# Kernel optimization log

Hardware: AMD Instinct MI355X
Metric: run time of the kernel (lower is better)

The kernel has to match this reference:

```python
import jax, jax.numpy as jnp
import numpy as np

K = 3  # number of nearest neighbors for interpolation
BIG = 1e10  # masks out cross-batch pairs in the distance matrix


def setup_inputs() -> dict:
    key = jax.random.key(0)
    ks = jax.random.split(key, 8)
    N, Ns, C, Cs, B = 4096, 16384, 256, 128, 4
    Din, H = C + Cs, 256
    return {
        "x": jax.random.normal(ks[0], (N, C), dtype=jnp.float32),
        "pos": jax.random.normal(ks[1], (N, 3), dtype=jnp.float32),
        "batch": jnp.sort(jax.random.randint(ks[2], (N,), 0, B)),
        "x_skip": jax.random.normal(ks[3], (Ns, Cs), dtype=jnp.float32),
        "pos_skip": jax.random.normal(ks[4], (Ns, 3), dtype=jnp.float32),
        "batch_skip": jnp.sort(jax.random.randint(ks[5], (Ns,), 0, B)),
        "W1": jax.random.normal(ks[6], (Din, H), dtype=jnp.float32) * (1.0 / np.sqrt(Din)),
        "b1": jnp.zeros((H,), dtype=jnp.float32),
        "W2": jax.random.normal(ks[7], (H, H), dtype=jnp.float32) * (1.0 / np.sqrt(H)),
        "b2": jnp.zeros((H,), dtype=jnp.float32),
    }


def reference(x, pos, batch, x_skip, pos_skip, batch_skip, W1, b1, W2, b2):
    # knn_interpolate: squared distances from each fine point to all coarse points,
    # masked so neighbors only come from the same batch element.
    d2 = jnp.sum((pos_skip[:, None, :] - pos[None, :, :]) ** 2, axis=-1)  # [Ns, N]
    d2 = jnp.where(batch_skip[:, None] != batch[None, :], BIG, d2)
    neg_d2, idx = jax.lax.top_k(-d2, K)          # k smallest distances, [Ns, K]
    w = 1.0 / jnp.clip(-neg_d2, 1e-16)           # inverse-squared-distance weights
    num = jnp.sum(x[idx] * w[..., None], axis=1)  # [Ns, C] weighted gather-reduce
    y = num / jnp.sum(w, axis=1, keepdims=True)
    # concat skip features, then MLP (Linear-ReLU-Linear-ReLU)
    y = jnp.concatenate([y, x_skip], axis=1)      # [Ns, C + Cs]
    h = jax.nn.relu(y @ W1 + b1)
    out = jax.nn.relu(h @ W2 + b2)
    return (out, pos_skip, batch_skip)
```

## Files before the change

kernel.cpp:

```cpp
#include <hip/hip_runtime.h>
#include <stdint.h>

#define NPTS   4096
#define NSKIP  16384
#define CCH    256
#define CSK    128
#define DIN    384
#define HDIM   256
#define BIGF   1e10f

typedef unsigned short u16;
typedef __attribute__((ext_vector_type(8))) short short8;
typedef __attribute__((ext_vector_type(4))) float floatx4;

__device__ __forceinline__ u16 f2bf(float f) {
    union { float f; uint32_t u; } c; c.f = f;
    uint32_t u = c.u;
    return (u16)((u + 0x7FFFu + ((u >> 16) & 1u)) >> 16);
}

__device__ __forceinline__ double pkkey(float d, int j) {
    return __hiloint2double(__float_as_int(d), j);
}

__global__ __launch_bounds__(256) void prep_kernel(
    const float* __restrict__ W1, const float* __restrict__ W2,
    u16* __restrict__ W1p, u16* __restrict__ W2p,
    const float* __restrict__ pos, float4* __restrict__ pos4,
    const int* __restrict__ batch, int* __restrict__ range)
{
    const int bid = blockIdx.x;
    const int t = threadIdx.x;

    const float* W = (bid < 48) ? W1 : W2;
    u16* Wp       = (bid < 48) ? W1p : W2p;
    const int KT  = (bid < 48) ? 12 : 8;
    const int g   = ((bid < 48) ? bid : (bid - 48)) * 256 + t;

    const int lane = g & 63;
    const int kt = (g >> 6) % KT;
    const int nt = (g >> 6) / KT;
    const int kbase = kt * 32 + (lane >> 4) * 8;
    const int n = nt * 16 + (lane & 15);
    u16 v[8];
#pragma unroll
    for (int j = 0; j < 8; ++j) v[j] = f2bf(W[(size_t)(kbase + j) * HDIM + n]);
#pragma unroll
    for (int j = 0; j < 8; ++j) Wp[(size_t)g * 8 + j] = v[j];

    if (bid >= 48 && bid < 64) {
        const int p = (bid - 48) * 256 + t;
        pos4[p] = make_float4(pos[p * 3 + 0], pos[p * 3 + 1], pos[p * 3 + 2], 0.0f);
    }

    if (bid == 0) {
        for (int j = t * 16; j < t * 16 + 16; ++j) {
            if (j == 0) {
                const int b0 = batch[0];
                for (int b = 0; b <= b0; ++b) range[b] = 0;
            } else {
                const int bp = batch[j - 1], bj = batch[j];
                for (int b = bp + 1; b <= bj; ++b) range[b] = j;
            }
            if (j == NPTS - 1) {
                const int bl = batch[NPTS - 1];
                for (int b = bl + 1; b <= 4; ++b) range[b] = NPTS;
            }
        }
    }
}

__global__ __launch_bounds__(256) void knn_kernel(
    const float4* __restrict__ pos4, const int* __restrict__ range,
    const float* __restrict__ pos_skip, const int* __restrict__ batch_skip,
    int* __restrict__ idx3, float* __restrict__ w3)
{
    const int t = threadIdx.x;
    const int i = blockIdx.x * 8 + (t >> 5);
    const int sub = t & 31;
    const int b = batch_skip[i];
    const int start = range[b], end = range[b + 1];

    const float px = pos_skip[i * 3 + 0];
    const float py = pos_skip[i * 3 + 1];
    const float pz = pos_skip[i * 3 + 2];

    const double BIGKEY = pkkey(BIGF, 0x7FFFFFFF);
    double k0 = BIGKEY, k1 = BIGKEY, k2 = BIGKEY;

    for (int j = start + sub; j < end; j += 32) {
        const float4 q = pos4[j];
        const float dx = __fsub_rn(px, q.x);
        const float dy = __fsub_rn(py, q.y);
        const float dz = __fsub_rn(pz, q.z);
        const float dd = __fadd_rn(__fadd_rn(__fmul_rn(dx, dx), __fmul_rn(dy, dy)),
                                   __fmul_rn(dz, dz));
        const double kk = pkkey(dd, j);
        const double u0 = fmax(k0, kk); k0 = fmin(k0, kk);
        const double u1 = fmax(k1, u0); k1 = fmin(k1, u0);
        k2 = fmin(k2, u1);
    }

#pragma unroll
    for (int m = 1; m < 32; m <<= 1) {
        const double o0 = __shfl_xor(k0, m);
        const double o1 = __shfl_xor(k1, m);
        const double o2 = __shfl_xor(k2, m);
        double u0 = fmax(k0, o0); k0 = fmin(k0, o0);
        double u1 = fmax(k1, u0); k1 = fmin(k1, u0);
        k2 = fmin(k2, u1);
        u1 = fmax(k1, o1); k1 = fmin(k1, o1);
        k2 = fmin(k2, u1);
        k2 = fmin(k2, o2);
    }

    if (sub == 0) {
        const float d0 = __int_as_float(__double2hiint(k0));
        const float d1 = __int_as_float(__double2hiint(k1));
        const float d2 = __int_as_float(__double2hiint(k2));
        const float w0 = 1.0f / fmaxf(d0, 1e-16f);
        const float w1 = 1.0f / fmaxf(d1, 1e-16f);
        const float w2 = 1.0f / fmaxf(d2, 1e-16f);
        const float inv = 1.0f / (w0 + w1 + w2);
        idx3[i * 3 + 0] = __double2loint(k0);
        idx3[i * 3 + 1] = __double2loint(k1);
        idx3[i * 3 + 2] = __double2loint(k2);
        w3[i * 3 + 0] = w0 * inv; w3[i * 3 + 1] = w1 * inv; w3[i * 3 + 2] = w2 * inv;
    }
}

__global__ __launch_bounds__(256) void fused_mlp_kernel(
    const float* __restrict__ x, const float* __restrict__ x_skip,
    const int* __restrict__ idx3, const float* __restrict__ w3,
    const u16* __restrict__ W1p, const float* __restrict__ b1,
    const u16* __restrict__ W2p, const float* __restrict__ b2,
    const float* __restrict__ pos_skip, const int* __restrict__ batch_skip,
    float* __restrict__ out)
{
    __shared__ u16 sA[32 * 392];
    const int t = threadIdx.x;
    const int row0 = blockIdx.x * 32;

#pragma unroll
    for (int k = 0; k < 8; ++k) {
        const int g = t + 256 * k;
        const int row = g >> 6, c4 = g & 63;
        const int R = row0 + row;
        const int i0 = idx3[R * 3 + 0], i1 = idx3[R * 3 + 1], i2 = idx3[R * 3 + 2];
        const float w0 = w3[R * 3 + 0], w1 = w3[R * 3 + 1], w2 = w3[R * 3 + 2];
        const float4 v0 = *(const float4*)(x + (size_t)i0 * CCH + c4 * 4);
        const float4 v1 = *(const float4*)(x + (size_t)i1 * CCH + c4 * 4);
        const float4 v2 = *(const float4*)(x + (size_t)i2 * CCH + c4 * 4);
        const float a  = w0 * v0.x + w1 * v1.x + w2 * v2.x;
        const float bq = w0 * v0.y + w1 * v1.y + w2 * v2.y;
        const float cq = w0 * v0.z + w1 * v1.z + w2 * v2.z;
        const float dq = w0 * v0.w + w1 * v1.w + w2 * v2.w;
        uint2 pk;
        pk.x = (uint32_t)f2bf(a)  | ((uint32_t)f2bf(bq) << 16);
        pk.y = (uint32_t)f2bf(cq) | ((uint32_t)f2bf(dq) << 16);
        *(uint2*)(sA + row * 392 + c4 * 4) = pk;
    }
#pragma unroll
    for (int k = 0; k < 4; ++k) {
        const int g = t + 256 * k;
        const int row = g >> 5, c4 = g & 31;
        const float4 v = *(const float4*)(x_skip + (size_t)(row0 + row) * CSK + c4 * 4);
        uint2 pk;
        pk.x = (uint32_t)f2bf(v.x) | ((uint32_t)f2bf(v.y) << 16);
        pk.y = (uint32_t)f2bf(v.z) | ((uint32_t)f2bf(v.w) << 16);
        *(uint2*)(sA + row * 392 + CCH + c4 * 4) = pk;
    }
    __syncthreads();

    const int wave = t >> 6, lane = t & 63;
    const int quad = lane >> 4, ml = lane & 15;

    floatx4 acc[2][4] = {};
    {
        const u16* aA = sA + ml * 392 + quad * 8;
        for (int kt = 0; kt < 12; ++kt) {
            short8 a0 = *(const short8*)(aA + kt * 32);
            short8 a1 = *(const short8*)(aA + 16 * 392 + kt * 32);
#pragma unroll
            for (int nt = 0; nt < 4; ++nt) {
                const int ntile = wave * 4 + nt;
                short8 bfr = *(const short8*)(W1p + (size_t)((ntile * 12 + kt) * 64 + lane) * 8);
                acc[0][nt] = __builtin_amdgcn_mfma_f32_16x16x32_bf16(a0, bfr, acc[0][nt], 0, 0, 0);
                acc[1][nt] = __builtin_amdgcn_mfma_f32_16x16x32_bf16(a1, bfr, acc[1][nt], 0, 0, 0);
            }
        }
    }
    __syncthreads();

#pragma unroll
    for (int mt = 0; mt < 2; ++mt) {
#pragma unroll
        for (int nt = 0; nt < 4; ++nt) {
            const int n = (wave * 4 + nt) * 16 + ml;
            const float bv = b1[n];
#pragma unroll
            for (int r = 0; r < 4; ++r) {
                const int m = mt * 16 + quad * 4 + r;
                sA[m * 264 + n] = f2bf(fmaxf(acc[mt][nt][r] + bv, 0.0f));
            }
        }
    }
    __syncthreads();

    floatx4 acc2[2][4] = {};
    {
        const u16* aH = sA + ml * 264 + quad * 8;
        for (int kt = 0; kt < 8; ++kt) {
            short8 a0 = *(const short8*)(aH + kt * 32);
            short8 a1 = *(const short8*)(aH + 16 * 264 + kt * 32);
#pragma unroll
            for (int nt = 0; nt < 4; ++nt) {
                const int ntile = wave * 4 + nt;
                short8 bfr = *(const short8*)(W2p + (size_t)((ntile * 8 + kt) * 64 + lane) * 8);
                acc2[0][nt] = __builtin_amdgcn_mfma_f32_16x16x32_bf16(a0, bfr, acc2[0][nt], 0, 0, 0);
                acc2[1][nt] = __builtin_amdgcn_mfma_f32_16x16x32_bf16(a1, bfr, acc2[1][nt], 0, 0, 0);
            }
        }
    }

#pragma unroll
    for (int mt = 0; mt < 2; ++mt) {
#pragma unroll
        for (int nt = 0; nt < 4; ++nt) {
            const int n = (wave * 4 + nt) * 16 + ml;
            const float bv = b2[n];
#pragma unroll
            for (int r = 0; r < 4; ++r) {
                const int m = row0 + mt * 16 + quad * 4 + r;
                out[(size_t)m * HDIM + n] = fmaxf(acc2[mt][nt][r] + bv, 0.0f);
            }
        }
    }

    if (t < 128) {
        const int e = blockIdx.x * 128 + t;
        const size_t base = (size_t)NSKIP * HDIM;
        if (e < NSKIP * 3) out[base + e] = pos_skip[e];
        else               out[base + e] = (float)batch_skip[e - NSKIP * 3];
    }
}

extern "C" void kernel_launch(void* const* d_in, const int* in_sizes, int n_in,
                              void* d_out, int out_size, void* d_ws, size_t ws_size,
                              hipStream_t stream) {
    const float* x         = (const float*)d_in[0];
    const float* pos       = (const float*)d_in[1];
    const int*   batch     = (const int*)d_in[2];
    const float* x_skip    = (const float*)d_in[3];
    const float* pos_skip  = (const float*)d_in[4];
    const int*   batch_skip= (const int*)d_in[5];
    const float* W1        = (const float*)d_in[6];
    const float* b1        = (const float*)d_in[7];
    const float* W2        = (const float*)d_in[8];
    const float* b2        = (const float*)d_in[9];
    float* out = (float*)d_out;

    char* ws = (char*)d_ws;
    u16*    W1p   = (u16*)ws;
    u16*    W2p   = (u16*)(ws + 196608);
    int*    range = (int*)(ws + 327680);
    float4* pos4  = (float4*)(ws + 327712);
    int*    idx3  = (int*)(ws + 393248);
    float*  w3    = (float*)(ws + 589856);

    prep_kernel<<<80, 256, 0, stream>>>(W1, W2, W1p, W2p, pos, pos4, batch, range);
    knn_kernel<<<NSKIP / 8, 256, 0, stream>>>(pos4, range, pos_skip, batch_skip, idx3, w3);
    fused_mlp_kernel<<<NSKIP / 32, 256, 0, stream>>>(x, x_skip, idx3, w3,
                                                     W1p, b1, W2p, b2,
                                                     pos_skip, batch_skip, out);
}
```

Before: 119.7 us.

## Fuse KNN search into MLP kernel with 8 lanes per query

Merges the separate KNN kernel into the fused MLP kernel: each block first finds the 3 nearest coarse points for its 32 rows using 8 lanes per row and stores indices and weights in shared memory, then gathers and runs the MLP. This removes one kernel launch and the global write/read of idx3 and w3. In exchange, each lane now scans four times as many candidates serially and the KNN phase runs with far fewer threads in flight, which may leave it latency-bound.

After: 137.8 us. 15.2% more time.

```diff
diff --git a/kernel.cpp b/kernel.cpp
--- a/kernel.cpp
+++ b/kernel.cpp
@@ -70,84 +70,95 @@
     }
 }
 
-__global__ __launch_bounds__(256) void knn_kernel(
+__global__ __launch_bounds__(256) void knn_fused_kernel(
+    const float* __restrict__ x, const float* __restrict__ x_skip,
     const float4* __restrict__ pos4, const int* __restrict__ range,
-    const float* __restrict__ pos_skip, const int* __restrict__ batch_skip,
-    int* __restrict__ idx3, float* __restrict__ w3)
-{
-    const int t = threadIdx.x;
-    const int i = blockIdx.x * 8 + (t >> 5);
-    const int sub = t & 31;
-    const int b = batch_skip[i];
-    const int start = range[b], end = range[b + 1];
-
-    const float px = pos_skip[i * 3 + 0];
-    const float py = pos_skip[i * 3 + 1];
-    const float pz = pos_skip[i * 3 + 2];
-
-    const double BIGKEY = pkkey(BIGF, 0x7FFFFFFF);
-    double k0 = BIGKEY, k1 = BIGKEY, k2 = BIGKEY;
-
-    for (int j = start + sub; j < end; j += 32) {
-        const float4 q = pos4[j];
-        const float dx = __fsub_rn(px, q.x);
-        const float dy = __fsub_rn(py, q.y);
-        const float dz = __fsub_rn(pz, q.z);
-        const float dd = __fadd_rn(__fadd_rn(__fmul_rn(dx, dx), __fmul_rn(dy, dy)),
-                                   __fmul_rn(dz, dz));
-        const double kk = pkkey(dd, j);
-        const double u0 = fmax(k0, kk); k0 = fmin(k0, kk);
-        const double u1 = fmax(k1, u0); k1 = fmin(k1, u0);
-        k2 = fmin(k2, u1);
-    }
-
-#pragma unroll
-    for (int m = 1; m < 32; m <<= 1) {
-        const double o0 = __shfl_xor(k0, m);
-        const double o1 = __shfl_xor(k1, m);
-        const double o2 = __shfl_xor(k2, m);
-        double u0 = fmax(k0, o0); k0 = fmin(k0, o0);
-        double u1 = fmax(k1, u0); k1 = fmin(k1, u0);
-        k2 = fmin(k2, u1);
-        u1 = fmax(k1, o1); k1 = fmin(k1, o1);
-        k2 = fmin(k2, u1);
-        k2 = fmin(k2, o2);
-    }
-
-    if (sub == 0) {
-        const float d0 = __int_as_float(__double2hiint(k0));
-        const float d1 = __int_as_float(__double2hiint(k1));
-        const float d2 = __int_as_float(__double2hiint(k2));
-        const float w0 = 1.0f / fmaxf(d0, 1e-16f);
-        const float w1 = 1.0f / fmaxf(d1, 1e-16f);
-        const float w2 = 1.0f / fmaxf(d2, 1e-16f);
-        const float inv = 1.0f / (w0 + w1 + w2);
-        idx3[i * 3 + 0] = __double2loint(k0);
-        idx3[i * 3 + 1] = __double2loint(k1);
-        idx3[i * 3 + 2] = __double2loint(k2);
-        w3[i * 3 + 0] = w0 * inv; w3[i * 3 + 1] = w1 * inv; w3[i * 3 + 2] = w2 * inv;
-    }
-}
-
-__global__ __launch_bounds__(256) void fused_mlp_kernel(
-    const float* __restrict__ x, const float* __restrict__ x_skip,
-    const int* __restrict__ idx3, const float* __restrict__ w3,
     const u16* __restrict__ W1p, const float* __restrict__ b1,
     const u16* __restrict__ W2p, const float* __restrict__ b2,
     const float* __restrict__ pos_skip, const int* __restrict__ batch_skip,
     float* __restrict__ out)
 {
     __shared__ u16 sA[32 * 392];
+    __shared__ int   sIdx[32 * 3];
+    __shared__ float sWgt[32 * 3];
     const int t = threadIdx.x;
     const int row0 = blockIdx.x * 32;
+
+#pragma unroll
+    for (int k = 0; k < 4; ++k) {
+        const int g = t + 256 * k;
+        const int row = g >> 5, c4 = g & 31;
+        const float4 v = *(const float4*)(x_skip + (size_t)(row0 + row) * CSK + c4 * 4);
+        uint2 pk;
+        pk.x = (uint32_t)f2bf(v.x) | ((uint32_t)f2bf(v.y) << 16);
+        pk.y = (uint32_t)f2bf(v.z) | ((uint32_t)f2bf(v.w) << 16);
+        *(uint2*)(sA + row * 392 + CCH + c4 * 4) = pk;
+    }
+
+    {
+        const int row_l = t >> 3;
+        const int sub   = t & 7;
+        const int i = row0 + row_l;
+        const int b = batch_skip[i];
+        const int start = range[b], end = range[b + 1];
+
+        const float px = pos_skip[i * 3 + 0];
+        const float py = pos_skip[i * 3 + 1];
+        const float pz = pos_skip[i * 3 + 2];
+
+        const double BIGKEY = pkkey(BIGF, 0x7FFFFFFF);
+        double k0 = BIGKEY, k1 = BIGKEY, k2 = BIGKEY;
+
+        for (int j = start + sub; j < end; j += 8) {
+            const float4 q = pos4[j];
+            const float dx = __fsub_rn(px, q.x);
+            const float dy = __fsub_rn(py, q.y);
+            const float dz = __fsub_rn(pz, q.z);
+            const float dd = __fadd_rn(__fadd_rn(__fmul_rn(dx, dx), __fmul_rn(dy, dy)),
+                                       __fmul_rn(dz, dz));
+            const double kk = pkkey(dd, j);
+            const double u0 = fmax(k0, kk); k0 = fmin(k0, kk);
+            const double u1 = fmax(k1, u0); k1 = fmin(k1, u0);
+            k2 = fmin(k2, u1);
+        }
+
+#pragma unroll
+        for (int m = 1; m < 8; m <<= 1) {
+            const double o0 = __shfl_xor(k0, m);
+            const double o1 = __shfl_xor(k1, m);
+            const double o2 = __shfl_xor(k2, m);
+            double u0 = fmax(k0, o0); k0 = fmin(k0, o0);
+            double u1 = fmax(k1, u0); k1 = fmin(k1, u0);
+            k2 = fmin(k2, u1);
+            u1 = fmax(k1, o1); k1 = fmin(k1, o1);
+            k2 = fmin(k2, u1);
+            k2 = fmin(k2, o2);
+        }
+
+        if (sub == 0) {
+            const float d0 = __int_as_float(__double2hiint(k0));
+            const float d1 = __int_as_float(__double2hiint(k1));
+            const float d2 = __int_as_float(__double2hiint(k2));
+            const float w0 = 1.0f / fmaxf(d0, 1e-16f);
+            const float w1 = 1.0f / fmaxf(d1, 1e-16f);
+            const float w2 = 1.0f / fmaxf(d2, 1e-16f);
+            const float inv = 1.0f / (w0 + w1 + w2);
+            sIdx[row_l * 3 + 0] = __double2loint(k0);
+            sIdx[row_l * 3 + 1] = __double2loint(k1);
+            sIdx[row_l * 3 + 2] = __double2loint(k2);
+            sWgt[row_l * 3 + 0] = w0 * inv;
+            sWgt[row_l * 3 + 1] = w1 * inv;
+            sWgt[row_l * 3 + 2] = w2 * inv;
+        }
+    }
+    __syncthreads();
 
 #pragma unroll
     for (int k = 0; k < 8; ++k) {
         const int g = t + 256 * k;
         const int row = g >> 6, c4 = g & 63;
-        const int R = row0 + row;
-        const int i0 = idx3[R * 3 + 0], i1 = idx3[R * 3 + 1], i2 = idx3[R * 3 + 2];
-        const float w0 = w3[R * 3 + 0], w1 = w3[R * 3 + 1], w2 = w3[R * 3 + 2];
+        const int i0 = sIdx[row * 3 + 0], i1 = sIdx[row * 3 + 1], i2 = sIdx[row * 3 + 2];
+        const float w0 = sWgt[row * 3 + 0], w1 = sWgt[row * 3 + 1], w2 = sWgt[row * 3 + 2];
         const float4 v0 = *(const float4*)(x + (size_t)i0 * CCH + c4 * 4);
         const float4 v1 = *(const float4*)(x + (size_t)i1 * CCH + c4 * 4);
         const float4 v2 = *(const float4*)(x + (size_t)i2 * CCH + c4 * 4);
@@ -159,16 +170,6 @@
         pk.x = (uint32_t)f2bf(a)  | ((uint32_t)f2bf(bq) << 16);
         pk.y = (uint32_t)f2bf(cq) | ((uint32_t)f2bf(dq) << 16);
         *(uint2*)(sA + row * 392 + c4 * 4) = pk;
-    }
-#pragma unroll
-    for (int k = 0; k < 4; ++k) {
-        const int g = t + 256 * k;
-        const int row = g >> 5, c4 = g & 31;
-        const float4 v = *(const float4*)(x_skip + (size_t)(row0 + row) * CSK + c4 * 4);
-        uint2 pk;
-        pk.x = (uint32_t)f2bf(v.x) | ((uint32_t)f2bf(v.y) << 16);
-        pk.y = (uint32_t)f2bf(v.z) | ((uint32_t)f2bf(v.w) << 16);
-        *(uint2*)(sA + row * 392 + CCH + c4 * 4) = pk;
     }
     __syncthreads();
 
@@ -265,12 +266,9 @@
     u16*    W2p   = (u16*)(ws + 196608);
     int*    range = (int*)(ws + 327680);
     float4* pos4  = (float4*)(ws + 327712);
-    int*    idx3  = (int*)(ws + 393248);
-    float*  w3    = (float*)(ws + 589856);
 
     prep_kernel<<<80, 256, 0, stream>>>(W1, W2, W1p, W2p, pos, pos4, batch, range);
-    knn_kernel<<<NSKIP / 8, 256, 0, stream>>>(pos4, range, pos_skip, batch_skip, idx3, w3);
-    fused_mlp_kernel<<<NSKIP / 32, 256, 0, stream>>>(x, x_skip, idx3, w3,
+    knn_fused_kernel<<<NSKIP / 32, 256, 0, stream>>>(x, x_skip, pos4, range,
                                                      W1p, b1, W2p, b2,
                                                      pos_skip, batch_skip, out);
 }
```

## Merge weight prep and kNN search into one kernel launch

Applied to the files above, without the earlier changes.

Folds the weight bf16 packing into the kNN kernel as 80 extra blocks, removing one launch and the dependency between the two kernels. Batch ranges are now found per block by binary search into shared memory, and pos is read directly as three scalar loads instead of from a padded float4 copy. This saves a launch, the serialization between the two kernels and the pos4 staging writes. In exchange, every kNN block repeats a small binary search and does unaligned scalar position loads.

Measured after the change: 118.0 us. About the same (-1.4%).

```diff
diff --git a/kernel.cpp b/kernel.cpp
--- a/kernel.cpp
+++ b/kernel.cpp
@@ -23,63 +23,50 @@
     return __hiloint2double(__float_as_int(d), j);
 }
 
-__global__ __launch_bounds__(256) void prep_kernel(
+__global__ __launch_bounds__(256) void prep_knn_kernel(
     const float* __restrict__ W1, const float* __restrict__ W2,
     u16* __restrict__ W1p, u16* __restrict__ W2p,
-    const float* __restrict__ pos, float4* __restrict__ pos4,
-    const int* __restrict__ batch, int* __restrict__ range)
+    const float* __restrict__ pos, const int* __restrict__ batch,
+    const float* __restrict__ pos_skip, const int* __restrict__ batch_skip,
+    int* __restrict__ idx3, float* __restrict__ w3)
 {
     const int bid = blockIdx.x;
     const int t = threadIdx.x;
 
-    const float* W = (bid < 48) ? W1 : W2;
-    u16* Wp       = (bid < 48) ? W1p : W2p;
-    const int KT  = (bid < 48) ? 12 : 8;
-    const int g   = ((bid < 48) ? bid : (bid - 48)) * 256 + t;
-
-    const int lane = g & 63;
-    const int kt = (g >> 6) % KT;
-    const int nt = (g >> 6) / KT;
-    const int kbase = kt * 32 + (lane >> 4) * 8;
-    const int n = nt * 16 + (lane & 15);
-    u16 v[8];
-#pragma unroll
-    for (int j = 0; j < 8; ++j) v[j] = f2bf(W[(size_t)(kbase + j) * HDIM + n]);
-#pragma unroll
-    for (int j = 0; j < 8; ++j) Wp[(size_t)g * 8 + j] = v[j];
-
-    if (bid >= 48 && bid < 64) {
-        const int p = (bid - 48) * 256 + t;
-        pos4[p] = make_float4(pos[p * 3 + 0], pos[p * 3 + 1], pos[p * 3 + 2], 0.0f);
-    }
-
-    if (bid == 0) {
-        for (int j = t * 16; j < t * 16 + 16; ++j) {
-            if (j == 0) {
-                const int b0 = batch[0];
-                for (int b = 0; b <= b0; ++b) range[b] = 0;
-            } else {
-                const int bp = batch[j - 1], bj = batch[j];
-                for (int b = bp + 1; b <= bj; ++b) range[b] = j;
-            }
-            if (j == NPTS - 1) {
-                const int bl = batch[NPTS - 1];
-                for (int b = bl + 1; b <= 4; ++b) range[b] = NPTS;
-            }
-        }
-    }
-}
-
-__global__ __launch_bounds__(256) void knn_kernel(
-    const float4* __restrict__ pos4, const int* __restrict__ range,
-    const float* __restrict__ pos_skip, const int* __restrict__ batch_skip,
-    int* __restrict__ idx3, float* __restrict__ w3)
-{
-    const int t = threadIdx.x;
-    const int i = blockIdx.x * 8 + (t >> 5);
+    if (bid < 80) {
+        const float* W = (bid < 48) ? W1 : W2;
+        u16* Wp       = (bid < 48) ? W1p : W2p;
+        const int KT  = (bid < 48) ? 12 : 8;
+        const int g   = ((bid < 48) ? bid : (bid - 48)) * 256 + t;
+
+        const int lane = g & 63;
+        const int kt = (g >> 6) % KT;
+        const int nt = (g >> 6) / KT;
+        const int kbase = kt * 32 + (lane >> 4) * 8;
+        const int n = nt * 16 + (lane & 15);
+        u16 v[8];
+#pragma unroll
+        for (int j = 0; j < 8; ++j) v[j] = f2bf(W[(size_t)(kbase + j) * HDIM + n]);
+#pragma unroll
+        for (int j = 0; j < 8; ++j) Wp[(size_t)g * 8 + j] = v[j];
+        return;
+    }
+
+    __shared__ int sRange[5];
+    if (t < 5) {
+        int lo = 0, hi = NPTS;
+        while (lo < hi) {
+            const int m = (lo + hi) >> 1;
+            if (batch[m] < t) lo = m + 1; else hi = m;
+        }
+        sRange[t] = lo;
+    }
+    __syncthreads();
+
+    const int i = (bid - 80) * 8 + (t >> 5);
     const int sub = t & 31;
     const int b = batch_skip[i];
-    const int start = range[b], end = range[b + 1];
+    const int start = sRange[b], end = sRange[b + 1];
 
     const float px = pos_skip[i * 3 + 0];
     const float py = pos_skip[i * 3 + 1];
@@ -89,10 +76,12 @@
     double k0 = BIGKEY, k1 = BIGKEY, k2 = BIGKEY;
 
     for (int j = start + sub; j < end; j += 32) {
-        const float4 q = pos4[j];
-        const float dx = __fsub_rn(px, q.x);
-        const float dy = __fsub_rn(py, q.y);
-        const float dz = __fsub_rn(pz, q.z);
+        const float qx = pos[j * 3 + 0];
+        const float qy = pos[j * 3 + 1];
+        const float qz = pos[j * 3 + 2];
+        const float dx = __fsub_rn(px, qx);
+        const float dy = __fsub_rn(py, qy);
+        const float dz = __fsub_rn(pz, qz);
         const float dd = __fadd_rn(__fadd_rn(__fmul_rn(dx, dx), __fmul_rn(dy, dy)),
                                    __fmul_rn(dz, dz));
         const double kk = pkkey(dd, j);
@@ -263,13 +252,13 @@
     char* ws = (char*)d_ws;
     u16*    W1p   = (u16*)ws;
     u16*    W2p   = (u16*)(ws + 196608);
-    int*    range = (int*)(ws + 327680);
-    float4* pos4  = (float4*)(ws + 327712);
-    int*    idx3  = (int*)(ws + 393248);
-    float*  w3    = (float*)(ws + 589856);
-
-    prep_kernel<<<80, 256, 0, stream>>>(W1, W2, W1p, W2p, pos, pos4, batch, range);
-    knn_kernel<<<NSKIP / 8, 256, 0, stream>>>(pos4, range, pos_skip, batch_skip, idx3, w3);
+    int*    idx3  = (int*)(ws + 327680);
+    float*  w3    = (float*)(ws + 524288);
+
+    prep_knn_kernel<<<80 + NSKIP / 8, 256, 0, stream>>>(W1, W2, W1p, W2p,
+                                                        pos, batch,
+                                                        pos_skip, batch_skip,
+                                                        idx3, w3);
     fused_mlp_kernel<<<NSKIP / 32, 256, 0, stream>>>(x, x_skip, idx3, w3,
                                                      W1p, b1, W2p, b2,
                                                      pos_skip, batch_skip, out);
```
